# Optimization experiments

Measured on AMD Instinct MI355X. Metric: run time of the kernel, lower is better.

Reference implementation:

```python
import jax, jax.numpy as jnp
import numpy as np
from jax import lax

HEADS = 4
K_DIM = 256
HALF = K_DIM // 2
KNN = 32
N_KEYS = 512
N_INDICES = N_KEYS * N_KEYS
D_MODEL = 1024
BS = 2048


def setup_inputs() -> dict:
    key = jax.random.key(0)
    k1, k2, k3, k4 = jax.random.split(key, 4)
    x = jax.random.normal(k1, (BS, D_MODEL), dtype=jnp.float32)
    # query net: Linear(d_model -> heads * k_dim)
    W_query = jax.random.normal(k2, (HEADS * K_DIM, D_MODEL), dtype=jnp.float32) / np.sqrt(D_MODEL)
    b_query = jnp.zeros((HEADS * K_DIM,), dtype=jnp.float32)
    # product sub-keys (shared between both halves: use_different_keys=False)
    keys = jax.random.normal(k3, (N_KEYS, HALF), dtype=jnp.float32) / np.sqrt(HALF)
    # memory values table
    values = jax.random.normal(k4, (N_INDICES, D_MODEL), dtype=jnp.float32) * 0.02
    return {"x": x, "W_query": W_query, "b_query": b_query, "keys": keys, "values": values}


def _pkm_forward(x, W_query, b_query, keys, values):
    bs = x.shape[0]
    # query net -> (bs*heads, k_dim)
    q = (x @ W_query.T + b_query).reshape(bs * HEADS, K_DIM)
    q1, q2 = q[:, :HALF], q[:, HALF:]
    # sub-key scores: (bs*heads, n_keys)
    s1 = q1 @ keys.T
    s2 = q2 @ keys.T
    s1, i1 = lax.top_k(s1, KNN)
    s2, i2 = lax.top_k(s2, KNN)
    # cartesian product of sub-scores / sub-indices: (bs*heads, knn*knn)
    all_scores = (s1[:, :, None] + s2[:, None, :]).reshape(-1, KNN * KNN)
    all_indices = (i1[:, :, None] * N_KEYS + i2[:, None, :]).reshape(-1, KNN * KNN)
    scores, best = lax.top_k(all_scores, KNN)            # (bs*heads, knn)
    indices = jnp.take_along_axis(all_indices, best, axis=1)
    # softmax over knn per head
    scores = jax.nn.softmax(scores, axis=-1)
    # merge heads: (bs, heads*knn)
    scores = scores.reshape(bs, HEADS * KNN)
    indices = indices.reshape(bs, HEADS * KNN)
    # EmbeddingBag(sum) with per-sample weights
    out = jnp.einsum('bk,bkd->bd', scores, values[indices])
    return out


def reference(x, W_query, b_query, keys, values):
    return _pkm_forward(x, W_query, b_query, keys, values)
```

## Files before the change

### kernel.cpp

```cpp
#include <hip/hip_runtime.h>

#define NROWS 8192
#define NKEYS 512
#define KNN   32

__global__ __launch_bounds__(256)
void gemm_nt_f32(const float* __restrict__ A, int lda,
                 const float* __restrict__ B, int ldb,
                 float* __restrict__ C, int ldc,
                 const float* __restrict__ bias, int K) {
  __shared__ float As[16][132];
  __shared__ float Bs[16][68];
  const int tid = threadIdx.x;
  const int tx = tid & 15;
  const int ty = tid >> 4;
  const int m0 = blockIdx.y * 128;
  const int n0 = blockIdx.x * 64;
  const int am = tid >> 1;
  const int ak = (tid & 1) * 8;
  const int bn = tid >> 2;
  const int bk = (tid & 3) * 4;

  float acc[8][4];
  #pragma unroll
  for (int i = 0; i < 8; i++)
    #pragma unroll
    for (int j = 0; j < 4; j++) acc[i][j] = 0.f;

  const float* Arow = A + (size_t)(m0 + am) * lda + ak;
  const float* Brow = B + (size_t)(n0 + bn) * ldb + bk;

  for (int kt = 0; kt < K; kt += 16) {
    float4 a0 = *(const float4*)(Arow + kt);
    float4 a1 = *(const float4*)(Arow + kt + 4);
    float4 b0 = *(const float4*)(Brow + kt);
    As[ak+0][am] = a0.x; As[ak+1][am] = a0.y; As[ak+2][am] = a0.z; As[ak+3][am] = a0.w;
    As[ak+4][am] = a1.x; As[ak+5][am] = a1.y; As[ak+6][am] = a1.z; As[ak+7][am] = a1.w;
    Bs[bk+0][bn] = b0.x; Bs[bk+1][bn] = b0.y; Bs[bk+2][bn] = b0.z; Bs[bk+3][bn] = b0.w;
    __syncthreads();
    #pragma unroll
    for (int k = 0; k < 16; k++) {
      float a[8], b[4];
      *(float4*)&a[0] = *(const float4*)&As[k][ty*8];
      *(float4*)&a[4] = *(const float4*)&As[k][ty*8+4];
      *(float4*)&b[0] = *(const float4*)&Bs[k][tx*4];
      #pragma unroll
      for (int i = 0; i < 8; i++)
        #pragma unroll
        for (int j = 0; j < 4; j++)
          acc[i][j] = fmaf(a[i], b[j], acc[i][j]);
    }
    __syncthreads();
  }

  float bv[4] = {0.f, 0.f, 0.f, 0.f};
  if (bias) {
    #pragma unroll
    for (int j = 0; j < 4; j++) bv[j] = bias[n0 + tx*4 + j];
  }
  #pragma unroll
  for (int i = 0; i < 8; i++) {
    float4 o;
    o.x = acc[i][0] + bv[0];
    o.y = acc[i][1] + bv[1];
    o.z = acc[i][2] + bv[2];
    o.w = acc[i][3] + bv[3];
    *(float4*)&C[(size_t)(m0 + ty*8 + i) * ldc + n0 + tx*4] = o;
  }
}

__global__ __launch_bounds__(256)
void topk512(const float* __restrict__ s1, const float* __restrict__ s2,
             float* __restrict__ v1, int* __restrict__ i1,
             float* __restrict__ v2, int* __restrict__ i2) {
  const int wid  = (int)((blockIdx.x * blockDim.x + threadIdx.x) >> 6);
  const int lane = threadIdx.x & 63;
  const float* src; float* dv; int* di;
  if (wid < NROWS) {
    src = s1 + (size_t)wid * NKEYS; dv = v1 + (size_t)wid * KNN; di = i1 + (size_t)wid * KNN;
  } else {
    int r = wid - NROWS;
    src = s2 + (size_t)r * NKEYS;  dv = v2 + (size_t)r * KNN;  di = i2 + (size_t)r * KNN;
  }
  float v[8];
  #pragma unroll
  for (int s = 0; s < 8; s++) v[s] = src[s*64 + lane];

  float outv = 0.f; int outi = 0;
  for (int round = 0; round < KNN; round++) {
    float m = v[0]; int ms = 0;
    #pragma unroll
    for (int s = 1; s < 8; s++) { if (v[s] > m) { m = v[s]; ms = s; } }
    int gi = ms*64 + lane;
    #pragma unroll
    for (int off = 32; off >= 1; off >>= 1) {
      float om = __shfl_xor(m, off, 64);
      int  ogi = __shfl_xor(gi, off, 64);
      if (om > m || (om == m && ogi < gi)) { m = om; gi = ogi; }
    }
    if (lane == round) { outv = m; outi = gi; }
    if ((gi & 63) == lane) {
      int s = gi >> 6;
      #pragma unroll
      for (int ss = 0; ss < 8; ss++) if (ss == s) v[ss] = -INFINITY;
    }
  }
  if (lane < KNN) { dv[lane] = outv; di[lane] = outi; }
}

__global__ __launch_bounds__(256)
void combine_topk(const float* __restrict__ v1, const int* __restrict__ i1,
                  const float* __restrict__ v2, const int* __restrict__ i2,
                  float* __restrict__ wout, int* __restrict__ idxout) {
  const int wid  = (int)((blockIdx.x * blockDim.x + threadIdx.x) >> 6);
  const int lane = threadIdx.x & 63;

  const float* a  = v1 + (size_t)wid * KNN;
  const int*   ai = i1 + (size_t)wid * KNN;
  const float* b  = v2 + (size_t)wid * KNN;
  const int*   bi = i2 + (size_t)wid * KNN;

  float cv[2]; int cidx[2];
  #pragma unroll
  for (int h = 0; h < 2; h++) {
    int t = lane + h*64;
    int i = 0, rem = t;
    while (i < 32 && rem >= 32/(i+1)) { rem -= 32/(i+1); i++; }
    if (i < 32) {
      float av = a[i], bvv = b[rem];
      cv[h]   = av + bvv;
      cidx[h] = ai[i] * NKEYS + bi[rem];
    } else {
      cv[h] = -INFINITY; cidx[h] = 0;
    }
  }

  #pragma unroll
  for (int k = 2; k <= 128; k <<= 1) {
    #pragma unroll
    for (int j = 64; j >= 1; j >>= 1) {
      if (j > (k >> 1)) continue;
      if (j >= 2) {
        int mdist = j >> 1;
        #pragma unroll
        for (int h = 0; h < 2; h++) {
          float ov = __shfl_xor(cv[h],   mdist, 64);
          int   oi = __shfl_xor(cidx[h], mdist, 64);
          int e = 2*lane + h;
          bool lower   = (lane & mdist) == 0;
          bool desc    = (e & k) == 0;
          bool keepmax = (lower == desc);
          bool take    = keepmax ? (ov > cv[h]) : (ov < cv[h]);
          if (take) { cv[h] = ov; cidx[h] = oi; }
        }
      } else {
        int e = 2*lane;
        bool desc = (e & k) == 0;
        bool sw = desc ? (cv[0] < cv[1]) : (cv[0] > cv[1]);
        if (sw) {
          float tv = cv[0]; cv[0] = cv[1]; cv[1] = tv;
          int  ti = cidx[0]; cidx[0] = cidx[1]; cidx[1] = ti;
        }
      }
    }
  }

  float mx = __shfl(cv[0], 0, 64);
  float e0 = (lane < 16) ? __expf(cv[0] - mx) : 0.f;
  float e1 = (lane < 16) ? __expf(cv[1] - mx) : 0.f;
  float ssum = e0 + e1;
  #pragma unroll
  for (int off = 32; off >= 1; off >>= 1) ssum += __shfl_xor(ssum, off, 64);

  if (lane < 16) {
    size_t base = (size_t)wid * KNN + 2*lane;
    wout[base]     = e0 / ssum;
    wout[base + 1] = e1 / ssum;
    idxout[base]     = cidx[0];
    idxout[base + 1] = cidx[1];
  }
}

__global__ __launch_bounds__(256)
void gather_wsum(const float* __restrict__ w, const int* __restrict__ idx,
                 const float* __restrict__ values, float* __restrict__ out) {
  const int b = blockIdx.x;
  const int t = threadIdx.x;
  __shared__ float sw[128];
  __shared__ int   si[128];
  if (t < 128) {
    sw[t] = w[(size_t)b*128 + t];
    si[t] = idx[(size_t)b*128 + t];
  }
  __syncthreads();
  const float4* V = (const float4*)values;
  float4 acc = make_float4(0.f, 0.f, 0.f, 0.f);
  #pragma unroll 8
  for (int k = 0; k < 128; k++) {
    float wk = sw[k];
    float4 v = V[(size_t)si[k] * 256 + t];
    acc.x = fmaf(wk, v.x, acc.x);
    acc.y = fmaf(wk, v.y, acc.y);
    acc.z = fmaf(wk, v.z, acc.z);
    acc.w = fmaf(wk, v.w, acc.w);
  }
  ((float4*)out)[(size_t)b*256 + t] = acc;
}

extern "C" void kernel_launch(void* const* d_in, const int* in_sizes, int n_in,
                              void* d_out, int out_size, void* d_ws, size_t ws_size,
                              hipStream_t stream) {
  const float* x      = (const float*)d_in[0];
  const float* Wq     = (const float*)d_in[1];
  const float* bq     = (const float*)d_in[2];
  const float* keys   = (const float*)d_in[3];
  const float* values = (const float*)d_in[4];
  float* out = (float*)d_out;

  char* ws = (char*)d_ws;
  float* q   = (float*)(ws);
  float* s1  = (float*)(ws + (8u  << 20));
  float* s2  = (float*)(ws + (24u << 20));
  float* v1  = (float*)(ws + (40u << 20));
  int*   i1  = (int*)  (ws + (41u << 20));
  float* v2  = (float*)(ws + (42u << 20));
  int*   i2  = (int*)  (ws + (43u << 20));
  float* wsc = (float*)(ws + (44u << 20));
  int*   fid = (int*)  (ws + (45u << 20));

  gemm_nt_f32<<<dim3(1024/64, 2048/128), 256, 0, stream>>>(x, 1024, Wq, 1024, q, 1024, bq, 1024);
  gemm_nt_f32<<<dim3(512/64, 8192/128), 256, 0, stream>>>(q,       256, keys, 128, s1, 512, nullptr, 128);
  gemm_nt_f32<<<dim3(512/64, 8192/128), 256, 0, stream>>>(q + 128, 256, keys, 128, s2, 512, nullptr, 128);
  topk512<<<4096, 256, 0, stream>>>(s1, s2, v1, i1, v2, i2);
  combine_topk<<<2048, 256, 0, stream>>>(v1, i1, v2, i2, wsc, fid);
  gather_wsum<<<2048, 256, 0, stream>>>(wsc, fid, values, out);
}
```

Measured before the change: 1.518 ms.

## Replace iterative top-k with radix threshold select; merge sub-key GEMMs; smaller query GEMM tiles

The 32-round argmax top-k over 512 scores is replaced by a bitwise radix search on order-preserving uint keys using ballot counts. It is followed by ballot-based compaction into shared memory and a 32-wide bitonic sort. The two sub-key score GEMMs become a single GEMM, by treating q as 16384 rows of 128 and interleaving the half1/half2 outputs. The query projection uses a new 64x64-tile GEMM variant to launch more blocks. The aim is to cut the serial shuffle-reduction rounds in top-k and one kernel launch, and to raise occupancy on the first GEMM. Tie handling at the threshold now keeps the lowest indices in compaction order.

```diff
diff --git a/kernel.cpp b/kernel.cpp
--- a/kernel.cpp
+++ b/kernel.cpp
@@ -70,42 +70,135 @@
 }
 
 __global__ __launch_bounds__(256)
-void topk512(const float* __restrict__ s1, const float* __restrict__ s2,
+void gemm_nt_f32_64(const float* __restrict__ A, int lda,
+                    const float* __restrict__ B, int ldb,
+                    float* __restrict__ C, int ldc,
+                    const float* __restrict__ bias, int K) {
+  __shared__ float As[16][68];
+  __shared__ float Bs[16][68];
+  const int tid = threadIdx.x;
+  const int tx = tid & 15;
+  const int ty = tid >> 4;
+  const int m0 = blockIdx.y * 64;
+  const int n0 = blockIdx.x * 64;
+  const int lm = tid >> 2;
+  const int lk = (tid & 3) * 4;
+
+  float acc[4][4];
+  #pragma unroll
+  for (int i = 0; i < 4; i++)
+    #pragma unroll
+    for (int j = 0; j < 4; j++) acc[i][j] = 0.f;
+
+  const float* Arow = A + (size_t)(m0 + lm) * lda + lk;
+  const float* Brow = B + (size_t)(n0 + lm) * ldb + lk;
+
+  for (int kt = 0; kt < K; kt += 16) {
+    float4 a0 = *(const float4*)(Arow + kt);
+    float4 b0 = *(const float4*)(Brow + kt);
+    As[lk+0][lm] = a0.x; As[lk+1][lm] = a0.y; As[lk+2][lm] = a0.z; As[lk+3][lm] = a0.w;
+    Bs[lk+0][lm] = b0.x; Bs[lk+1][lm] = b0.y; Bs[lk+2][lm] = b0.z; Bs[lk+3][lm] = b0.w;
+    __syncthreads();
+    #pragma unroll
+    for (int k = 0; k < 16; k++) {
+      float a[4], b[4];
+      *(float4*)&a[0] = *(const float4*)&As[k][ty*4];
+      *(float4*)&b[0] = *(const float4*)&Bs[k][tx*4];
+      #pragma unroll
+      for (int i = 0; i < 4; i++)
+        #pragma unroll
+        for (int j = 0; j < 4; j++)
+          acc[i][j] = fmaf(a[i], b[j], acc[i][j]);
+    }
+    __syncthreads();
+  }
+
+  float bv[4] = {0.f, 0.f, 0.f, 0.f};
+  if (bias) {
+    #pragma unroll
+    for (int j = 0; j < 4; j++) bv[j] = bias[n0 + tx*4 + j];
+  }
+  #pragma unroll
+  for (int i = 0; i < 4; i++) {
+    float4 o;
+    o.x = acc[i][0] + bv[0];
+    o.y = acc[i][1] + bv[1];
+    o.z = acc[i][2] + bv[2];
+    o.w = acc[i][3] + bv[3];
+    *(float4*)&C[(size_t)(m0 + ty*4 + i) * ldc + n0 + tx*4] = o;
+  }
+}
+
+__global__ __launch_bounds__(256)
+void topk512(const float* __restrict__ s,
              float* __restrict__ v1, int* __restrict__ i1,
              float* __restrict__ v2, int* __restrict__ i2) {
   const int wid  = (int)((blockIdx.x * blockDim.x + threadIdx.x) >> 6);
   const int lane = threadIdx.x & 63;
-  const float* src; float* dv; int* di;
-  if (wid < NROWS) {
-    src = s1 + (size_t)wid * NKEYS; dv = v1 + (size_t)wid * KNN; di = i1 + (size_t)wid * KNN;
-  } else {
-    int r = wid - NROWS;
-    src = s2 + (size_t)r * NKEYS;  dv = v2 + (size_t)r * KNN;  di = i2 + (size_t)r * KNN;
-  }
-  float v[8];
-  #pragma unroll
-  for (int s = 0; s < 8; s++) v[s] = src[s*64 + lane];
-
-  float outv = 0.f; int outi = 0;
-  for (int round = 0; round < KNN; round++) {
-    float m = v[0]; int ms = 0;
-    #pragma unroll
-    for (int s = 1; s < 8; s++) { if (v[s] > m) { m = v[s]; ms = s; } }
-    int gi = ms*64 + lane;
-    #pragma unroll
-    for (int off = 32; off >= 1; off >>= 1) {
-      float om = __shfl_xor(m, off, 64);
-      int  ogi = __shfl_xor(gi, off, 64);
-      if (om > m || (om == m && ogi < gi)) { m = om; gi = ogi; }
-    }
-    if (lane == round) { outv = m; outi = gi; }
-    if ((gi & 63) == lane) {
-      int s = gi >> 6;
-      #pragma unroll
-      for (int ss = 0; ss < 8; ss++) if (ss == s) v[ss] = -INFINITY;
-    }
-  }
-  if (lane < KNN) { dv[lane] = outv; di[lane] = outi; }
+  const int wv   = threadIdx.x >> 6;
+  const float* src = s + (size_t)wid * NKEYS;
+  const int row = wid >> 1;
+  float* dv = ((wid & 1) ? v2 : v1) + (size_t)row * KNN;
+  int*   di = ((wid & 1) ? i2 : i1) + (size_t)row * KNN;
+
+  float v[8]; unsigned u[8];
+  #pragma unroll
+  for (int k8 = 0; k8 < 8; k8++) {
+    float f = src[k8*64 + lane];
+    v[k8] = f;
+    unsigned b = __float_as_uint(f);
+    u[k8] = (b & 0x80000000u) ? ~b : (b | 0x80000000u);
+  }
+
+  unsigned T = 0u;
+  for (int bit = 31; bit >= 0; bit--) {
+    unsigned cand = T | (1u << bit);
+    int cnt = 0;
+    #pragma unroll
+    for (int k8 = 0; k8 < 8; k8++)
+      cnt += __popcll(__ballot(u[k8] >= cand));
+    if (cnt >= KNN) T = cand;
+  }
+
+  __shared__ float cval[4][KNN];
+  __shared__ int   cidx[4][KNN];
+  const unsigned long long lt = (1ull << lane) - 1ull;
+  int base = 0;
+  #pragma unroll
+  for (int k8 = 0; k8 < 8; k8++) {
+    unsigned long long m = __ballot(u[k8] > T);
+    if (u[k8] > T) {
+      int p = base + __popcll(m & lt);
+      cval[wv][p] = v[k8];
+      cidx[wv][p] = k8*64 + lane;
+    }
+    base += __popcll(m);
+  }
+  #pragma unroll
+  for (int k8 = 0; k8 < 8; k8++) {
+    unsigned long long m = __ballot(u[k8] == T);
+    if (u[k8] == T) {
+      int p = base + __popcll(m & lt);
+      if (p < KNN) { cval[wv][p] = v[k8]; cidx[wv][p] = k8*64 + lane; }
+    }
+    base += __popcll(m);
+  }
+  __syncthreads();
+
+  float sv = (lane < KNN) ? cval[wv][lane] : -INFINITY;
+  int   sx = (lane < KNN) ? cidx[wv][lane] : 0x7fffffff;
+  #pragma unroll
+  for (int k = 2; k <= KNN; k <<= 1) {
+    #pragma unroll
+    for (int j = k >> 1; j >= 1; j >>= 1) {
+      float ov = __shfl_xor(sv, j, 64);
+      int   ox = __shfl_xor(sx, j, 64);
+      bool keepmax = (((lane & j) == 0) == ((lane & k) == 0));
+      bool ogt = (ov > sv) || (ov == sv && ox < sx);
+      if (keepmax ? ogt : !ogt) { sv = ov; sx = ox; }
+    }
+  }
+  if (lane < KNN) { dv[lane] = sv; di[lane] = sx; }
 }
 
 __global__ __launch_bounds__(256)
@@ -219,8 +312,7 @@
 
   char* ws = (char*)d_ws;
   float* q   = (float*)(ws);
-  float* s1  = (float*)(ws + (8u  << 20));
-  float* s2  = (float*)(ws + (24u << 20));
+  float* s   = (float*)(ws + (8u  << 20));
   float* v1  = (float*)(ws + (40u << 20));
   int*   i1  = (int*)  (ws + (41u << 20));
   float* v2  = (float*)(ws + (42u << 20));
@@ -228,10 +320,9 @@
   float* wsc = (float*)(ws + (44u << 20));
   int*   fid = (int*)  (ws + (45u << 20));
 
-  gemm_nt_f32<<<dim3(1024/64, 2048/128), 256, 0, stream>>>(x, 1024, Wq, 1024, q, 1024, bq, 1024);
-  gemm_nt_f32<<<dim3(512/64, 8192/128), 256, 0, stream>>>(q,       256, keys, 128, s1, 512, nullptr, 128);
-  gemm_nt_f32<<<dim3(512/64, 8192/128), 256, 0, stream>>>(q + 128, 256, keys, 128, s2, 512, nullptr, 128);
-  topk512<<<4096, 256, 0, stream>>>(s1, s2, v1, i1, v2, i2);
+  gemm_nt_f32_64<<<dim3(1024/64, 2048/64), 256, 0, stream>>>(x, 1024, Wq, 1024, q, 1024, bq, 1024);
+  gemm_nt_f32<<<dim3(512/64, 16384/128), 256, 0, stream>>>(q, 128, keys, 128, s, 512, nullptr, 128);
+  topk512<<<4096, 256, 0, stream>>>(s, v1, i1, v2, i2);
   combine_topk<<<2048, 256, 0, stream>>>(v1, i1, v2, i2, wsc, fid);
   gather_wsum<<<2048, 256, 0, stream>>>(wsc, fid, values, out);
 }
```

New measurement: 1.450 ms. 4.4% less time.
